# Kernel tuning notes

Measured on AMD Instinct MI355X. Metric: run time of the kernel, lower is better.

Reference implementation:

```python
import jax, jax.numpy as jnp
import numpy as np

LAYERS = 3       # opt.layer
B = 4096         # batch of sessions
MAX_LEN = 200    # padded session length
N_ITEMS = 100000 # item vocab (index 0 is PAD after zero-row concat)
E = 112          # emb_size (SessConv default)
EPS = 1e-12      # F.normalize eps


def setup_inputs() -> dict:
    key = jax.random.key(0)
    k0, k1, k2, k3, k4 = jax.random.split(key, 5)
    item_embedding = jax.random.normal(k0, (N_ITEMS, E), dtype=jnp.float32) * 0.1
    # Session-session adjacency A and diagonal inverse-degree D (so D @ A is row-normalized)
    A = jax.random.uniform(k1, (B, B), dtype=jnp.float32)
    D = jnp.diag(1.0 / A.sum(axis=1))
    # Padded session item indices; 0 == PAD row (zeros prepended to the table)
    session_item = jax.random.randint(k2, (B, MAX_LEN), 0, N_ITEMS + 1, dtype=jnp.int64)
    session_len = jax.random.randint(k3, (B, 1), 1, MAX_LEN + 1).astype(jnp.float32)
    # layers x Linear(E, E, bias=False) weights, torch layout [out, in]
    Ws = jax.random.normal(k4, (LAYERS, E, E), dtype=jnp.float32) * (1.0 / np.sqrt(E))
    return {"item_embedding": item_embedding, "D": D, "A": A,
            "session_len": session_len, "Ws": Ws, "session_item": session_item}


def reference(item_embedding, D, A, session_len, Ws, session_item):
    # Prepend zero row so index 0 gathers zeros (padding)
    emb = jnp.concatenate([jnp.zeros((1, E), item_embedding.dtype), item_embedding], axis=0)
    # Fused ragged gather + mean-pool (replaces per-session index_select + cpu/numpy roundtrip)
    seq_h = emb[session_item]                       # [B, MAX_LEN, E]
    session_emb = seq_h.sum(axis=1) / session_len   # [B, E]
    DA = D @ A                                      # [B, B]
    acc = session_emb                               # layer-0 term of the final average
    for i in range(LAYERS):
        session_emb = session_emb @ Ws[i].T         # Linear(E,E,bias=False)
        session_emb = DA @ session_emb              # session graph propagation
        nrm = jnp.linalg.norm(session_emb, axis=-1, keepdims=True)
        acc = acc + session_emb / jnp.maximum(nrm, EPS)  # appended term is L2-normalized
        # NOTE: next layer consumes the UN-normalized session_emb (as in the torch code)
    return acc / (LAYERS + 1)
```

## Files before the change

kernel.cpp:

```cpp
#include <hip/hip_runtime.h>
#include <hip/hip_bf16.h>

#define BSZ 4096
#define MAXLEN 200
#define EDIM 112
#define NKC 16

typedef __attribute__((ext_vector_type(8))) short bf16x8;
typedef __attribute__((ext_vector_type(4))) float f32x4;

static __device__ __forceinline__ short f2bf(float f) {
    unsigned u = __float_as_uint(f);
    unsigned r = (u + 0x7fffu + ((u >> 16) & 1u)) >> 16;
    return (short)r;
}
static __device__ __forceinline__ float bf2f(short s) {
    return __uint_as_float(((unsigned)(unsigned short)s) << 16);
}
static __device__ __forceinline__ bf16x8 cvt8(float4 a, float4 b) {
    bf16x8 r;
    r[0] = f2bf(a.x); r[1] = f2bf(a.y); r[2] = f2bf(a.z); r[3] = f2bf(a.w);
    r[4] = f2bf(b.x); r[5] = f2bf(b.y); r[6] = f2bf(b.z); r[7] = f2bf(b.w);
    return r;
}
static __device__ __forceinline__ unsigned pack2(float a, float b) {
    return ((unsigned)f2bf(a) & 0xffffu) | ((unsigned)f2bf(b) << 16);
}

__global__ __launch_bounds__(256) void f32_to_bf16(const float* __restrict__ src,
                                                   unsigned short* __restrict__ dst,
                                                   int ngroups, int zgroups) {
    int g = blockIdx.x * 256 + threadIdx.x;
    if (g >= ngroups) return;
    bf16x8 o;
    if (g < zgroups) {
        #pragma unroll
        for (int i = 0; i < 8; ++i) o[i] = 0;
    } else {
        const float* p = src + (size_t)(g - zgroups) * 8;
        float4 a = *(const float4*)p;
        float4 b = *(const float4*)(p + 4);
        o = cvt8(a, b);
    }
    *(bf16x8*)(dst + (size_t)g * 8) = o;
}

__global__ __launch_bounds__(256) void gather_pool_bf(const unsigned short* __restrict__ Ebf,
                                                      const int* __restrict__ items,
                                                      const float* __restrict__ slen,
                                                      float* __restrict__ S,
                                                      float* __restrict__ acc) {
    __shared__ float part[16][14][8];
    int wave = threadIdx.x >> 6;
    int lane = threadIdx.x & 63;
    int b = blockIdx.x;
    int rg = lane / 14;
    int c  = lane % 14;
    const int* it = items + (size_t)b * MAXLEN + wave * 50;
    float a[8];
    #pragma unroll
    for (int e = 0; e < 8; ++e) a[e] = 0.f;
    if (lane < 56) {
        #pragma unroll
        for (int t = 0; t < 13; ++t) {
            int j = t * 4 + rg;
            int idx = 0;
            if (j < 50) idx = it[j];
            bf16x8 v = *(const bf16x8*)(Ebf + (size_t)idx * EDIM + c * 8);
            #pragma unroll
            for (int e = 0; e < 8; ++e) a[e] += bf2f(v[e]);
        }
        #pragma unroll
        for (int e = 0; e < 8; ++e) part[wave * 4 + rg][c][e] = a[e];
    }
    __syncthreads();
    int tid = threadIdx.x;
    if (tid < EDIM) {
        int cc = tid >> 3, ee = tid & 7;
        float s = 0.f;
        #pragma unroll
        for (int g = 0; g < 16; ++g) s += part[g][cc][ee];
        s /= slen[b];
        S[(size_t)b * EDIM + tid]   = s;
        acc[(size_t)b * EDIM + tid] = s;
    }
}

static __device__ __forceinline__ bf16x8 ldcvt(const float* p, bool valid) {
    if (valid) {
        float4 a = *(const float4*)p;
        float4 b = *(const float4*)(p + 4);
        return cvt8(a, b);
    }
    bf16x8 z;
    #pragma unroll
    for (int i = 0; i < 8; ++i) z[i] = 0;
    return z;
}

template <int MODE>
__global__ __launch_bounds__(64, 4) void fused_mid(const float* __restrict__ Sin,
                                                   const float* __restrict__ Yp,
                                                   const float* __restrict__ Dm,
                                                   float* __restrict__ accb,
                                                   const float* __restrict__ W,
                                                   unsigned short* __restrict__ Bsw) {
    __shared__ unsigned short Ylds[16][136];
    int lane = threadIdx.x;
    int gw = blockIdx.x;
    int j0 = gw * 16;
    int nrow = lane & 15;
    int quad = lane >> 4;
    int ses = j0 + nrow;

    float4 v[7];
    if (MODE == 0) {
        const float4* p = (const float4*)(Sin + (size_t)ses * EDIM + quad * 28);
        #pragma unroll
        for (int i = 0; i < 7; ++i) v[i] = p[i];
    } else {
        #pragma unroll
        for (int i = 0; i < 7; ++i) v[i] = make_float4(0.f, 0.f, 0.f, 0.f);
        #pragma unroll 4
        for (int pp = 0; pp < NKC; ++pp) {
            const float4* p = (const float4*)(Yp + (size_t)pp * BSZ * EDIM
                                              + (size_t)ses * EDIM + quad * 28);
            #pragma unroll
            for (int i = 0; i < 7; ++i) {
                float4 t = p[i];
                v[i].x += t.x; v[i].y += t.y; v[i].z += t.z; v[i].w += t.w;
            }
        }
        float d = Dm[(size_t)ses * (BSZ + 1)];
        float ss = 0.f;
        #pragma unroll
        for (int i = 0; i < 7; ++i) {
            v[i].x *= d; v[i].y *= d; v[i].z *= d; v[i].w *= d;
            ss += v[i].x * v[i].x + v[i].y * v[i].y + v[i].z * v[i].z + v[i].w * v[i].w;
        }
        ss += __shfl_xor(ss, 16, 64);
        ss += __shfl_xor(ss, 32, 64);
        float rinv = 1.f / fmaxf(sqrtf(ss), 1e-12f);
        float4* pa = (float4*)(accb + (size_t)ses * EDIM + quad * 28);
        #pragma unroll
        for (int i = 0; i < 7; ++i) {
            float4 a = pa[i];
            a.x += v[i].x * rinv; a.y += v[i].y * rinv;
            a.z += v[i].z * rinv; a.w += v[i].w * rinv;
            pa[i] = a;
        }
    }

    #pragma unroll
    for (int i = 0; i < 7; ++i) {
        uint2 pk;
        pk.x = pack2(v[i].x, v[i].y);
        pk.y = pack2(v[i].z, v[i].w);
        *(uint2*)&Ylds[nrow][quad * 28 + i * 4] = pk;
    }
    *(uint2*)&Ylds[nrow][112 + quad * 4] = make_uint2(0u, 0u);
    __syncthreads();

    bf16x8 aF[4];
    #pragma unroll
    for (int k32 = 0; k32 < 4; ++k32)
        aF[k32] = *(bf16x8*)&Ylds[nrow][k32 * 32 + quad * 8];

    f32x4 acc[7];
    #pragma unroll
    for (int t = 0; t < 7; ++t) acc[t] = (f32x4){0.f, 0.f, 0.f, 0.f};
    #pragma unroll
    for (int t = 0; t < 7; ++t) {
        const float* wr = W + (size_t)(16 * t + nrow) * EDIM;
        #pragma unroll
        for (int k32 = 0; k32 < 4; ++k32) {
            bf16x8 bF = ldcvt(wr + k32 * 32 + quad * 8, (k32 < 3) || (quad < 2));
            acc[t] = __builtin_amdgcn_mfma_f32_16x16x32_bf16(aF[k32], bF, acc[t], 0, 0, 0);
        }
    }

    int k32f = j0 >> 5;
    int qp = ((j0 >> 4) & 1) * 2 + (quad >> 1);
    int e0 = (quad & 1) * 4;
    #pragma unroll
    for (int t = 0; t < 7; ++t) {
        uint2 pk;
        pk.x = pack2(acc[t][0], acc[t][1]);
        pk.y = pack2(acc[t][2], acc[t][3]);
        *(uint2*)(Bsw + ((size_t)(k32f * 7 + t) * 64 + qp * 16 + nrow) * 8 + e0) = pk;
    }
}

template <int AMODE>
__global__ __launch_bounds__(64, 4) void big_gemm(const float* __restrict__ Af,
                                                  unsigned short* __restrict__ Asw,
                                                  const unsigned short* __restrict__ Bsw,
                                                  float* __restrict__ Yp) {
    int lane = threadIdx.x;
    int mt2 = blockIdx.x & 127;
    int kc = blockIdx.x >> 7;
    int nrow = lane & 15;
    int quad = lane >> 4;

    f32x4 acc[2][7];
    #pragma unroll
    for (int s = 0; s < 2; ++s)
        #pragma unroll
        for (int t = 0; t < 7; ++t) acc[s][t] = (f32x4){0.f, 0.f, 0.f, 0.f};

    for (int ks = 0; ks < 8; ++ks) {
        int k32 = kc * 8 + ks;
        bf16x8 aF[2];
        #pragma unroll
        for (int sub = 0; sub < 2; ++sub) {
            int mtile = mt2 * 2 + sub;
            size_t afrag = ((size_t)(mtile * 128 + k32) * 64 + lane) * 8;
            if (AMODE == 0) {
                const float* p = Af + (size_t)(mtile * 16 + nrow) * 4096 + k32 * 32 + quad * 8;
                float4 a0 = *(const float4*)p;
                float4 a1 = *(const float4*)(p + 4);
                aF[sub] = cvt8(a0, a1);
                *(bf16x8*)(Asw + afrag) = aF[sub];
            } else {
                aF[sub] = *(const bf16x8*)(Asw + afrag);
            }
        }
        const unsigned short* bb = Bsw + ((size_t)k32 * 7 * 64 + lane) * 8;
        #pragma unroll
        for (int t = 0; t < 7; ++t) {
            bf16x8 bF = *(const bf16x8*)(bb + (size_t)t * 512);
            acc[0][t] = __builtin_amdgcn_mfma_f32_16x16x32_bf16(aF[0], bF, acc[0][t], 0, 0, 0);
            acc[1][t] = __builtin_amdgcn_mfma_f32_16x16x32_bf16(aF[1], bF, acc[1][t], 0, 0, 0);
        }
    }

    float* dst = Yp + (size_t)kc * BSZ * EDIM + (size_t)mt2 * 32 * EDIM;
    #pragma unroll
    for (int sub = 0; sub < 2; ++sub)
        #pragma unroll
        for (int t = 0; t < 7; ++t)
            #pragma unroll
            for (int r = 0; r < 4; ++r)
                dst[(size_t)(sub * 16 + quad * 4 + r) * EDIM + 16 * t + nrow] = acc[sub][t][r];
}

__global__ __launch_bounds__(256) void final_epilogue(const float* __restrict__ Yp,
                                                      const float* __restrict__ Dm,
                                                      const float* __restrict__ accb,
                                                      float* __restrict__ out) {
    int wave = threadIdx.x >> 6;
    int lane = threadIdx.x & 63;
    int b = blockIdx.x * 4 + wave;

    float2 v = make_float2(0.f, 0.f);
    size_t o2 = (size_t)b * 56 + lane;
    if (lane < 56) {
        #pragma unroll 4
        for (int p = 0; p < NKC; ++p) {
            float2 t = ((const float2*)(Yp + (size_t)p * BSZ * EDIM))[o2];
            v.x += t.x;
            v.y += t.y;
        }
    }
    float d = Dm[(size_t)b * (BSZ + 1)];
    v.x *= d; v.y *= d;
    float ss = v.x * v.x + v.y * v.y;
    #pragma unroll
    for (int off = 32; off; off >>= 1) ss += __shfl_xor(ss, off, 64);
    float nrm = fmaxf(sqrtf(ss), 1e-12f);
    if (lane < 56) {
        float2 a = ((const float2*)accb)[o2];
        ((float2*)out)[o2] = make_float2((a.x + v.x / nrm) * 0.25f,
                                         (a.y + v.y / nrm) * 0.25f);
    }
}

extern "C" void kernel_launch(void* const* d_in, const int* in_sizes, int n_in,
                              void* d_out, int out_size, void* d_ws, size_t ws_size,
                              hipStream_t stream) {
    (void)in_sizes; (void)n_in; (void)out_size; (void)ws_size;
    const float* emb   = (const float*)d_in[0];
    const float* Dm    = (const float*)d_in[1];
    const float* A     = (const float*)d_in[2];
    const float* slen  = (const float*)d_in[3];
    const float* Ws    = (const float*)d_in[4];
    const int*   items = (const int*)d_in[5];
    float* out = (float*)d_out;

    char* w = (char*)d_ws;
    float* Sa   = (float*)w;
    float* accb = Sa + BSZ * EDIM;
    float* Yp   = accb + BSZ * EDIM;
    unsigned short* Bsw = (unsigned short*)(Yp + (size_t)NKC * BSZ * EDIM);
    unsigned short* Ebf = Bsw + 128 * 7 * 64 * 8;
    unsigned short* Asw = Ebf + 100001 * EDIM;

    f32_to_bf16<<<5470, 256, 0, stream>>>(emb, Ebf, 1400014, 14);
    gather_pool_bf<<<BSZ, 256, 0, stream>>>(Ebf, items, slen, Sa, accb);
    fused_mid<0><<<256, 64, 0, stream>>>(Sa, nullptr, nullptr, nullptr, Ws, Bsw);
    big_gemm<0><<<2048, 64, 0, stream>>>(A, Asw, Bsw, Yp);
    fused_mid<1><<<256, 64, 0, stream>>>(nullptr, Yp, Dm, accb,
                                         Ws + (size_t)EDIM * EDIM, Bsw);
    big_gemm<1><<<2048, 64, 0, stream>>>(nullptr, Asw, Bsw, Yp);
    fused_mid<1><<<256, 64, 0, stream>>>(nullptr, Yp, Dm, accb,
                                         Ws + (size_t)2 * EDIM * EDIM, Bsw);
    big_gemm<1><<<2048, 64, 0, stream>>>(nullptr, Asw, Bsw, Yp);
    final_epilogue<<<BSZ / 4, 256, 0, stream>>>(Yp, Dm, accb, out);
}
```

Measured before the change: 287.9 us.

## Split A bf16 conversion into its own kernel and retile big_gemm to 256-thread blocks

Moves the fp32-to-bf16 swizzled conversion of A out of the first GEMM into a separate conv_A kernel that runs before the gather. All three GEMMs now use one kernel shape: four waves per 256-thread block, each wave computing a single 16-row M tile for its own K chunk. This gives more parallelism per launch and a uniform path. In exchange, each wave reuses a B fragment across one M tile instead of two, so B traffic per MFMA doubles. There is also one extra launch, plus a write and re-read of the converted A.

New measurement: 294.5 us. +2.3%, slower.

```diff
diff --git a/kernel.cpp b/kernel.cpp
--- a/kernel.cpp
+++ b/kernel.cpp
@@ -43,6 +43,25 @@
         o = cvt8(a, b);
     }
     *(bf16x8*)(dst + (size_t)g * 8) = o;
+}
+
+__global__ __launch_bounds__(256) void conv_A(const float* __restrict__ Af,
+                                              unsigned short* __restrict__ Asw) {
+    int wave = threadIdx.x >> 6;
+    int lane = threadIdx.x & 63;
+    int mtile = blockIdx.x & 255;
+    int kg = (blockIdx.x >> 8) * 4 + wave;
+    int nrow = lane & 15;
+    int quad = lane >> 4;
+    const float* row = Af + (size_t)(mtile * 16 + nrow) * 4096;
+    #pragma unroll
+    for (int i = 0; i < 4; ++i) {
+        int k32 = kg * 4 + i;
+        const float* p = row + k32 * 32 + quad * 8;
+        float4 a0 = *(const float4*)p;
+        float4 a1 = *(const float4*)(p + 4);
+        *(bf16x8*)(Asw + ((size_t)(mtile * 128 + k32) * 64 + lane) * 8) = cvt8(a0, a1);
+    }
 }
 
 __global__ __launch_bounds__(256) void gather_pool_bf(const unsigned short* __restrict__ Ebf,
@@ -191,57 +210,38 @@
     }
 }
 
-template <int AMODE>
-__global__ __launch_bounds__(64, 4) void big_gemm(const float* __restrict__ Af,
-                                                  unsigned short* __restrict__ Asw,
-                                                  const unsigned short* __restrict__ Bsw,
-                                                  float* __restrict__ Yp) {
-    int lane = threadIdx.x;
-    int mt2 = blockIdx.x & 127;
-    int kc = blockIdx.x >> 7;
+__global__ __launch_bounds__(256, 4) void big_gemm(const unsigned short* __restrict__ Asw,
+                                                   const unsigned short* __restrict__ Bsw,
+                                                   float* __restrict__ Yp) {
+    int wave = threadIdx.x >> 6;
+    int lane = threadIdx.x & 63;
+    int mtile = blockIdx.x & 255;
+    int kc = (blockIdx.x >> 8) * 4 + wave;
     int nrow = lane & 15;
     int quad = lane >> 4;
 
-    f32x4 acc[2][7];
-    #pragma unroll
-    for (int s = 0; s < 2; ++s)
-        #pragma unroll
-        for (int t = 0; t < 7; ++t) acc[s][t] = (f32x4){0.f, 0.f, 0.f, 0.f};
-
+    f32x4 acc[7];
+    #pragma unroll
+    for (int t = 0; t < 7; ++t) acc[t] = (f32x4){0.f, 0.f, 0.f, 0.f};
+
+    #pragma unroll
     for (int ks = 0; ks < 8; ++ks) {
         int k32 = kc * 8 + ks;
-        bf16x8 aF[2];
-        #pragma unroll
-        for (int sub = 0; sub < 2; ++sub) {
-            int mtile = mt2 * 2 + sub;
-            size_t afrag = ((size_t)(mtile * 128 + k32) * 64 + lane) * 8;
-            if (AMODE == 0) {
-                const float* p = Af + (size_t)(mtile * 16 + nrow) * 4096 + k32 * 32 + quad * 8;
-                float4 a0 = *(const float4*)p;
-                float4 a1 = *(const float4*)(p + 4);
-                aF[sub] = cvt8(a0, a1);
-                *(bf16x8*)(Asw + afrag) = aF[sub];
-            } else {
-                aF[sub] = *(const bf16x8*)(Asw + afrag);
-            }
-        }
+        bf16x8 aF = *(const bf16x8*)(Asw + ((size_t)(mtile * 128 + k32) * 64 + lane) * 8);
         const unsigned short* bb = Bsw + ((size_t)k32 * 7 * 64 + lane) * 8;
         #pragma unroll
         for (int t = 0; t < 7; ++t) {
             bf16x8 bF = *(const bf16x8*)(bb + (size_t)t * 512);
-            acc[0][t] = __builtin_amdgcn_mfma_f32_16x16x32_bf16(aF[0], bF, acc[0][t], 0, 0, 0);
-            acc[1][t] = __builtin_amdgcn_mfma_f32_16x16x32_bf16(aF[1], bF, acc[1][t], 0, 0, 0);
-        }
-    }
-
-    float* dst = Yp + (size_t)kc * BSZ * EDIM + (size_t)mt2 * 32 * EDIM;
-    #pragma unroll
-    for (int sub = 0; sub < 2; ++sub)
-        #pragma unroll
-        for (int t = 0; t < 7; ++t)
-            #pragma unroll
-            for (int r = 0; r < 4; ++r)
-                dst[(size_t)(sub * 16 + quad * 4 + r) * EDIM + 16 * t + nrow] = acc[sub][t][r];
+            acc[t] = __builtin_amdgcn_mfma_f32_16x16x32_bf16(aF, bF, acc[t], 0, 0, 0);
+        }
+    }
+
+    float* dst = Yp + (size_t)kc * BSZ * EDIM + (size_t)mtile * 16 * EDIM;
+    #pragma unroll
+    for (int t = 0; t < 7; ++t)
+        #pragma unroll
+        for (int r = 0; r < 4; ++r)
+            dst[(size_t)(quad * 4 + r) * EDIM + 16 * t + nrow] = acc[t][r];
 }
 
 __global__ __launch_bounds__(256) void final_epilogue(const float* __restrict__ Yp,
@@ -296,14 +296,15 @@
     unsigned short* Asw = Ebf + 100001 * EDIM;
 
     f32_to_bf16<<<5470, 256, 0, stream>>>(emb, Ebf, 1400014, 14);
+    conv_A<<<2048, 256, 0, stream>>>(A, Asw);
     gather_pool_bf<<<BSZ, 256, 0, stream>>>(Ebf, items, slen, Sa, accb);
     fused_mid<0><<<256, 64, 0, stream>>>(Sa, nullptr, nullptr, nullptr, Ws, Bsw);
-    big_gemm<0><<<2048, 64, 0, stream>>>(A, Asw, Bsw, Yp);
+    big_gemm<<<1024, 256, 0, stream>>>(Asw, Bsw, Yp);
     fused_mid<1><<<256, 64, 0, stream>>>(nullptr, Yp, Dm, accb,
                                          Ws + (size_t)EDIM * EDIM, Bsw);
-    big_gemm<1><<<2048, 64, 0, stream>>>(nullptr, Asw, Bsw, Yp);
+    big_gemm<<<1024, 256, 0, stream>>>(Asw, Bsw, Yp);
     fused_mid<1><<<256, 64, 0, stream>>>(nullptr, Yp, Dm, accb,
                                          Ws + (size_t)2 * EDIM * EDIM, Bsw);
-    big_gemm<1><<<2048, 64, 0, stream>>>(nullptr, Asw, Bsw, Yp);
+    big_gemm<<<1024, 256, 0, stream>>>(Asw, Bsw, Yp);
     final_epilogue<<<BSZ / 4, 256, 0, stream>>>(Yp, Dm, accb, out);
 }
```
